# Kernel optimization log

Hardware: AMD Instinct MI355X
Metric: run time of the kernel (lower is better)

Reference implementation:

```python
import jax, jax.numpy as jnp
import numpy as np

NUM_HEADS = 8
KEY_DIM = 512      # total projected dim across heads
VALUE_DIM = 512
EMBED_DIM = 512


def setup_inputs() -> dict:
    key = jax.random.key(0)
    ks = jax.random.split(key, 12)
    B, S, E = 8, 1024, EMBED_DIM
    sc_in = 1.0 / np.sqrt(E)
    sc_o = 1.0 / np.sqrt(KEY_DIM)
    return {
        "queries": jax.random.normal(ks[0], (B, S, E), jnp.float32),
        "keys": jax.random.normal(ks[1], (B, S, E), jnp.float32),
        "values": jax.random.normal(ks[2], (B, S, E), jnp.float32),
        "Wq": jax.random.normal(ks[3], (E, KEY_DIM), jnp.float32) * sc_in,
        "bq": jnp.zeros((KEY_DIM,), jnp.float32),
        "Wk": jax.random.normal(ks[4], (E, KEY_DIM), jnp.float32) * sc_in,
        "bk": jnp.zeros((KEY_DIM,), jnp.float32),
        "Wv": jax.random.normal(ks[5], (E, VALUE_DIM), jnp.float32) * sc_in,
        "bv": jnp.zeros((VALUE_DIM,), jnp.float32),
        "Wo": jax.random.normal(ks[6], (KEY_DIM, EMBED_DIM), jnp.float32) * sc_o,
        "bo": jnp.zeros((EMBED_DIM,), jnp.float32),
    }


def _split_heads(x):
    # [B, S, key_dim] -> [B, H, S, key_dim//H]
    B, S, D = x.shape
    return x.reshape(B, S, NUM_HEADS, D // NUM_HEADS).transpose(0, 2, 1, 3)


def reference(queries, keys, values, Wq, bq, Wk, bk, Wv, bv, Wo, bo):
    q = _split_heads(queries @ Wq + bq)   # [B,H,S,dh]
    k = _split_heads(keys @ Wk + bk)
    v = _split_heads(values @ Wv + bv)
    # NOTE: original scales by sqrt(full key_dim), not per-head dim
    scores = jnp.einsum("bhqd,bhkd->bhqk", q, k) / jnp.sqrt(
        jnp.asarray(KEY_DIM, jnp.float32))
    weights = jax.nn.softmax(scores, axis=-1)
    o = jnp.einsum("bhqk,bhkd->bhqd", weights, v)  # [B,H,S,dh]
    B, H, S, dh = o.shape
    o = o.transpose(0, 2, 1, 3).reshape(B, S, H * dh)  # merge heads -> key_dim
    return o @ Wo + bo
```

## Files before the change

kernel.cpp:

```cpp
#include <hip/hip_runtime.h>


typedef __bf16 bf16x8 __attribute__((ext_vector_type(8)));
typedef __bf16 bf16x4 __attribute__((ext_vector_type(4)));
typedef float  f32x4  __attribute__((ext_vector_type(4)));

#define MFMA(a, b, c) __builtin_amdgcn_mfma_f32_16x16x32_bf16((a), (b), (c), 0, 0, 0)

#define WAITN_BAR(N) asm volatile("s_waitcnt vmcnt(" #N ")\n\ts_barrier" ::: "memory")

__device__ inline bf16x8 cvt8(const float* p) {
  f32x4 u = *(const f32x4*)p;
  f32x4 v = *(const f32x4*)(p + 4);
  bf16x8 r;
  r[0] = (__bf16)u[0]; r[1] = (__bf16)u[1]; r[2] = (__bf16)u[2]; r[3] = (__bf16)u[3];
  r[4] = (__bf16)v[0]; r[5] = (__bf16)v[1]; r[6] = (__bf16)v[2]; r[7] = (__bf16)v[3];
  return r;
}

__device__ inline void gl_lds(const __bf16* g, __bf16* l) {
  __builtin_amdgcn_global_load_lds((const __attribute__((address_space(1))) void*)g,
                                   (__attribute__((address_space(3))) void*)l, 16, 0, 0);
}

__global__ __launch_bounds__(256) void cvt_qkv(const float* __restrict__ Q,
                                               const float* __restrict__ K,
                                               const float* __restrict__ V,
                                               __bf16* __restrict__ Qo,
                                               __bf16* __restrict__ Ko,
                                               __bf16* __restrict__ Vo) {
  const float* src;
  __bf16* dst;
  switch (blockIdx.y) {
    case 0: src = Q; dst = Qo; break;
    case 1: src = K; dst = Ko; break;
    default: src = V; dst = Vo; break;
  }
  const long idx = ((long)blockIdx.x * 256 + threadIdx.x) * 8;
  *(bf16x8*)(dst + idx) = cvt8(src + idx);
}

__global__ __launch_bounds__(256) void transpose_w4(const float* __restrict__ W0,
                                                    const float* __restrict__ W1,
                                                    const float* __restrict__ W2,
                                                    const float* __restrict__ W3,
                                                    __bf16* __restrict__ O0,
                                                    __bf16* __restrict__ O1,
                                                    __bf16* __restrict__ O2,
                                                    __bf16* __restrict__ O3,
                                                    float s0) {
  const float* in;
  __bf16* out;
  float sc = 1.0f;
  switch (blockIdx.y) {
    case 0: in = W0; out = O0; sc = s0; break;
    case 1: in = W1; out = O1; break;
    case 2: in = W2; out = O2; break;
    default: in = W3; out = O3; break;
  }
  __shared__ __align__(16) float t[64][65];
  const int tk = (blockIdx.x & 7) * 64;
  const int tn = (blockIdx.x >> 3) * 64;
  const int r0 = threadIdx.x >> 4;
  const int c4 = threadIdx.x & 15;
#pragma unroll
  for (int i = 0; i < 4; ++i) {
    int r = r0 + i * 16;
    f32x4 v = *(const f32x4*)(in + (long)(tk + r) * 512 + tn + c4 * 4);
#pragma unroll
    for (int j = 0; j < 4; ++j) t[r][c4 * 4 + j] = v[j] * sc;
  }
  __syncthreads();
  const int n0 = threadIdx.x >> 3;
  const int k8 = threadIdx.x & 7;
#pragma unroll
  for (int i = 0; i < 2; ++i) {
    int n = n0 + i * 32;
    bf16x8 v;
#pragma unroll
    for (int j = 0; j < 8; ++j) v[j] = (__bf16)t[k8 * 8 + j][n];
    *(bf16x8*)(out + (long)(tn + n) * 512 + tk + k8 * 8) = v;
  }
}

template <int MODE, typename OT>
__device__ __forceinline__ void gemm_core(const __bf16* __restrict__ X,
                                          const __bf16* __restrict__ Wt,
                                          const float* __restrict__ bias,
                                          OT* __restrict__ out, float bsc,
                                          char* smem) {
  __bf16* At = (__bf16*)smem;
  __bf16* Bt = (__bf16*)(smem + 24576);

  const int tid = threadIdx.x;
  const int lane = tid & 63, wid = tid >> 6, quad = lane >> 4, l16 = lane & 15;
  const int i = blockIdx.x;
  const int kk = i >> 3;
  const int bm = ((i & 7) * 8 + (kk >> 2)) * 128;
  const int bn = (kk & 3) * 128;
  const int wm = (wid >> 1) * 64;
  const int wn = (wid & 1) * 64;

  f32x4 acc[4][4] = {};

  const int rowB = lane >> 2;
  const int gB = (lane & 3) ^ ((rowB >> 1) & 3);

  auto stage = [&](int off, int k0) {
#pragma unroll
    for (int j = 0; j < 2; ++j) {
      const int g = wid * 2 + j;
      gl_lds(X + (long)(bm + g * 16 + rowB) * 512 + k0 + (gB << 3),
             &At[off + g * 512 + lane * 8]);
      gl_lds(Wt + (long)(bn + g * 16 + rowB) * 512 + k0 + (gB << 3),
             &Bt[off + g * 512 + lane * 8]);
    }
  };

  const int posm = quad ^ ((l16 >> 1) & 3);

  auto compute = [&](int co) {
    bf16x8 a[4], b[4];
#pragma unroll
    for (int t = 0; t < 4; ++t) {
      a[t] = *(const bf16x8*)(&At[co + (wm + t * 16 + l16) * 32 + (posm << 3)]);
      b[t] = *(const bf16x8*)(&Bt[co + (wn + t * 16 + l16) * 32 + (posm << 3)]);
    }
#pragma unroll
    for (int mt = 0; mt < 4; ++mt)
#pragma unroll
      for (int nt = 0; nt < 4; ++nt) acc[mt][nt] = MFMA(a[mt], b[nt], acc[mt][nt]);
  };

  stage(0, 0);
  stage(4096, 32);

  int co = 0, so = 8192;
  for (int c = 0; c < 15; ++c) {
    WAITN_BAR(4);
    if (c < 14) stage(so, (c + 2) * 32);
    compute(co);
    const int nc = 12288 - co - so;
    so = co;
    co = nc;
  }
  WAITN_BAR(0);
  compute(co);

  if constexpr (MODE == 4) {
    __syncthreads();
    __bf16* tb = (__bf16*)smem;
#pragma unroll
    for (int nt = 0; nt < 4; ++nt) {
      const int n = wn + nt * 16 + l16;
      const float bvv = bias[bn + n] * bsc;
#pragma unroll
      for (int mt = 0; mt < 4; ++mt) {
        const int m0 = wm + mt * 16 + quad * 4;
        bf16x4 w;
#pragma unroll
        for (int r = 0; r < 4; ++r) w[r] = (__bf16)(acc[mt][nt][r] + bvv);
        *(bf16x4*)(&tb[n * 128 + (((m0 >> 3) ^ (n & 15)) << 3) + (m0 & 7)]) = w;
      }
    }
    __syncthreads();
    const int nn = tid & 127, mhalf = tid >> 7;
    const int d = nn & 63, h = (bn + nn) >> 6;
    const int bb = bm >> 10;
    OT* ob = out + (long)(bb * 8 + h) * 65536;
#pragma unroll
    for (int gi = 0; gi < 8; ++gi) {
      const int gl = mhalf * 8 + gi;
      bf16x8 v = *(const bf16x8*)(&tb[nn * 128 + ((gl ^ (nn & 15)) << 3)]);
      const int cidx = ((bm & 1023) + (gl << 3)) >> 6;
      *(bf16x8*)(ob + cidx * 4096 + d * 64 + ((gi ^ (d & 7)) << 3)) = v;
    }
    return;
  }

#pragma unroll
  for (int nt = 0; nt < 4; ++nt) {
    const int n = bn + wn + nt * 16 + l16;
    const float bvv = bias[n] * bsc;
    const int h = n >> 6, d = n & 63;
#pragma unroll
    for (int mt = 0; mt < 4; ++mt) {
#pragma unroll
      for (int r = 0; r < 4; ++r) {
        const int m = bm + wm + mt * 16 + quad * 4 + r;
        const float v = acc[mt][nt][r] + bvv;
        if constexpr (MODE == 0) {
          out[(long)m * 512 + n] = (OT)v;
        } else if constexpr (MODE == 1) {
          const int bb = m >> 10, s = m & 1023;
          out[((long)((bb * 8 + h) * 1024 + s)) * 64 + d] = (OT)v;
        } else {
          const int bb = m >> 10, s = m & 1023;
          const long idx = (long)(bb * 8 + h) * 65536 + (s >> 6) * 4096 +
                           (s & 63) * 64 + (((d >> 3) ^ (s & 7)) << 3) + (d & 7);
          out[idx] = (OT)v;
        }
      }
    }
  }
}

__global__ __launch_bounds__(256) void gemm_qkv(
    const __bf16* __restrict__ Qx, const __bf16* __restrict__ Kx,
    const __bf16* __restrict__ Vx, const __bf16* __restrict__ Wqt,
    const __bf16* __restrict__ Wkt, const __bf16* __restrict__ Wvt,
    const float* __restrict__ bq, const float* __restrict__ bk,
    const float* __restrict__ bv, __bf16* __restrict__ Qp,
    __bf16* __restrict__ Kp, __bf16* __restrict__ Vtp, float qscale) {
  __shared__ __align__(16) char smem[49152];
  if (blockIdx.y == 0)
    gemm_core<1, __bf16>(Qx, Wqt, bq, Qp, qscale, smem);
  else if (blockIdx.y == 1)
    gemm_core<3, __bf16>(Kx, Wkt, bk, Kp, 1.0f, smem);
  else
    gemm_core<4, __bf16>(Vx, Wvt, bv, Vtp, 1.0f, smem);
}

__global__ __launch_bounds__(256) void gemm_o(const __bf16* __restrict__ Oc,
                                              const __bf16* __restrict__ Wot,
                                              const float* __restrict__ bo,
                                              float* __restrict__ out) {
  __shared__ __align__(16) char smem[49152];
  gemm_core<0, float>(Oc, Wot, bo, out, 1.0f, smem);
}

__global__ __launch_bounds__(256) void attn(const __bf16* __restrict__ Q,
                                            const __bf16* __restrict__ K,
                                            const __bf16* __restrict__ Vt,
                                            __bf16* __restrict__ Oc) {
  __shared__ __align__(16) __bf16 kbuf[12288];
  __shared__ __align__(16) __bf16 vbuf[12288];
  __shared__ __align__(16) __bf16 plds[4][2048];

  const int tid = threadIdx.x;
  const int lane = tid & 63, wid = tid >> 6, quad = lane >> 4, l16 = lane & 15;
  const int i = blockIdx.x;
  const int pair = (i & 7) + (((i >> 6) & 7) << 3);
  const int qt = (i >> 3) & 7;
  const int q0 = qt * 128 + wid * 32;
  const int b = pair >> 3, h = pair & 7;
  const int swz = l16 & 7;

  const __bf16* Qb = Q + (long)pair * 65536;
  const __bf16* Kb = K + (long)pair * 65536;
  const __bf16* Vb = Vt + (long)pair * 65536;
  __bf16* pw = plds[wid];

  bf16x8 bq[2][2];
#pragma unroll
  for (int t = 0; t < 2; ++t)
#pragma unroll
    for (int e = 0; e < 2; ++e)
      bq[t][e] = *(const bf16x8*)(Qb + (q0 + t * 16 + l16) * 64 + e * 32 + quad * 8);
  asm volatile("s_waitcnt vmcnt(0)" ::: "memory");

  float lr[2] = {0.f, 0.f};
  f32x4 oa[2][4] = {};

  auto stage = [&](int off, int c_) {
    const __bf16* kg = Kb + c_ * 4096 + tid * 8;
    const __bf16* vg = Vb + c_ * 4096 + tid * 8;
    gl_lds(kg, &kbuf[off + tid * 8]);
    gl_lds(kg + 2048, &kbuf[off + 2048 + tid * 8]);
    gl_lds(vg, &vbuf[off + tid * 8]);
    gl_lds(vg + 2048, &vbuf[off + 2048 + tid * 8]);
  };

  auto body = [&](int co) {
    f32x4 s[2][4] = {};
#pragma unroll
    for (int kt = 0; kt < 4; ++kt) {
      const int krow = co + (kt * 16 + l16) * 64;
      bf16x8 a0 = *(const bf16x8*)(&kbuf[krow + ((quad ^ swz) << 3)]);
      bf16x8 a1 = *(const bf16x8*)(&kbuf[krow + (((4 + quad) ^ swz) << 3)]);
#pragma unroll
      for (int t = 0; t < 2; ++t) {
        s[t][kt] = MFMA(a0, bq[t][0], s[t][kt]);
        s[t][kt] = MFMA(a1, bq[t][1], s[t][kt]);
      }
    }

#pragma unroll
    for (int t = 0; t < 2; ++t) {
      const int prow = (t * 16 + l16) * 64;
#pragma unroll
      for (int kt = 0; kt < 4; ++kt) {
        bf16x4 w;
#pragma unroll
        for (int r = 0; r < 4; ++r) {
          const float p = exp2f(s[t][kt][r]);
          lr[t] += p;
          w[r] = (__bf16)p;
        }
        *(bf16x4*)(&pw[prow + (((kt * 2 + (quad >> 1)) ^ swz) << 3) + (quad & 1) * 4]) = w;
      }
    }
    bf16x8 pb[2][2];
#pragma unroll
    for (int t = 0; t < 2; ++t)
#pragma unroll
      for (int e = 0; e < 2; ++e)
        pb[t][e] = *(const bf16x8*)(&pw[(t * 16 + l16) * 64 + (((e * 4 + quad) ^ swz) << 3)]);

#pragma unroll
    for (int nt = 0; nt < 4; ++nt) {
      const int drow = co + (nt * 16 + l16) * 64;
      bf16x8 v0 = *(const bf16x8*)(&vbuf[drow + ((quad ^ swz) << 3)]);
      bf16x8 v1 = *(const bf16x8*)(&vbuf[drow + (((4 + quad) ^ swz) << 3)]);
#pragma unroll
      for (int t = 0; t < 2; ++t) {
        oa[t][nt] = MFMA(v0, pb[t][0], oa[t][nt]);
        oa[t][nt] = MFMA(v1, pb[t][1], oa[t][nt]);
      }
    }
  };

  stage(0, 0);
  stage(4096, 1);

  int co = 0, so = 8192;
  for (int c = 0; c < 15; ++c) {
    WAITN_BAR(4);
    if (c < 14) stage(so, c + 2);
    body(co);
    const int nc = 12288 - co - so;
    so = co;
    co = nc;
  }
  WAITN_BAR(0);
  body(co);

#pragma unroll
  for (int t = 0; t < 2; ++t) {
    lr[t] += __shfl_xor(lr[t], 16);
    lr[t] += __shfl_xor(lr[t], 32);
    const float inv = 1.0f / lr[t];
    const long base = ((long)b * 1024 + q0 + t * 16 + l16) * 512 + h * 64 + quad * 4;
#pragma unroll
    for (int nt = 0; nt < 4; ++nt) {
      bf16x4 w;
#pragma unroll
      for (int r = 0; r < 4; ++r) w[r] = (__bf16)(oa[t][nt][r] * inv);
      *(bf16x4*)(Oc + base + nt * 16) = w;
    }
  }
}

extern "C" void kernel_launch(void* const* d_in, const int* in_sizes, int n_in,
                              void* d_out, int out_size, void* d_ws, size_t ws_size,
                              hipStream_t stream) {
  const float* queries = (const float*)d_in[0];
  const float* keys = (const float*)d_in[1];
  const float* values = (const float*)d_in[2];
  const float* Wq = (const float*)d_in[3];
  const float* bq = (const float*)d_in[4];
  const float* Wk = (const float*)d_in[5];
  const float* bk = (const float*)d_in[6];
  const float* Wv = (const float*)d_in[7];
  const float* bv = (const float*)d_in[8];
  const float* Wo = (const float*)d_in[9];
  const float* bo = (const float*)d_in[10];
  float* out = (float*)d_out;

  __bf16* ws = (__bf16*)d_ws;
  const long WSZ = 512 * 512;
  const long XSZ = 8192L * 512;
  __bf16* Wqt = ws;
  __bf16* Wkt = ws + WSZ;
  __bf16* Wvt = ws + 2 * WSZ;
  __bf16* Wot = ws + 3 * WSZ;
  __bf16* Qp = ws + 4 * WSZ;
  __bf16* Kp = Qp + XSZ;
  __bf16* Vtp = Kp + XSZ;
  __bf16* Oc = Vtp + XSZ;
  __bf16* Qbf = Oc + XSZ;
  __bf16* Kbf = Qbf + XSZ;
  __bf16* Vbf = Kbf + XSZ;

  const float qscale = 0.044194173824159216f * 1.4426950408889634f;

  cvt_qkv<<<dim3(2048, 3), 256, 0, stream>>>(queries, keys, values, Qbf, Kbf, Vbf);
  transpose_w4<<<dim3(64, 4), 256, 0, stream>>>(Wq, Wk, Wv, Wo, Wqt, Wkt, Wvt, Wot,
                                                qscale);

  gemm_qkv<<<dim3(256, 3), 256, 0, stream>>>(Qbf, Kbf, Vbf, Wqt, Wkt, Wvt,
                                             bq, bk, bv, Qp, Kp, Vtp, qscale);

  attn<<<512, 256, 0, stream>>>(Qp, Kp, Vtp, Oc);

  gemm_o<<<256, 256, 0, stream>>>(Oc, Wot, bo, out);
}
```

Measured before the change: 181.6 us.

## Store K/V in MFMA fragment layout and load directly to registers in attention

The K and V projection epilogues now write data pre-arranged in MFMA fragment order, so each lane can read its operand fragments from global memory with contiguous 16-byte loads. The attention kernel drops the LDS staging, the barriers and the triple buffering for K/V, and instead double-buffers K fragments in registers and loads V per chunk. It also uses the raw v_exp_f32 instruction, vector row-sum accumulators, s_setprio around MFMA blocks, and a launch bound of two blocks per CU. The cost is more register pressure, and every wave reads K/V from global or L2 on its own, with no sharing through LDS across the block.

```diff
diff --git a/kernel.cpp b/kernel.cpp
--- a/kernel.cpp
+++ b/kernel.cpp
@@ -8,6 +8,12 @@
 #define MFMA(a, b, c) __builtin_amdgcn_mfma_f32_16x16x32_bf16((a), (b), (c), 0, 0, 0)
 
 #define WAITN_BAR(N) asm volatile("s_waitcnt vmcnt(" #N ")\n\ts_barrier" ::: "memory")
+
+__device__ inline float fast_exp2(float x) {
+  float r;
+  asm("v_exp_f32 %0, %1" : "=v"(r) : "v"(x));
+  return r;
+}
 
 __device__ inline bf16x8 cvt8(const float* p) {
   f32x4 u = *(const f32x4*)p;
@@ -165,15 +171,17 @@
     }
     __syncthreads();
     const int nn = tid & 127, mhalf = tid >> 7;
-    const int d = nn & 63, h = (bn + nn) >> 6;
+    const int h = (bn + nn) >> 6;
     const int bb = bm >> 10;
     OT* ob = out + (long)(bb * 8 + h) * 65536;
+    const int cbase = (bm & 1023) >> 6;
 #pragma unroll
     for (int gi = 0; gi < 8; ++gi) {
       const int gl = mhalf * 8 + gi;
       bf16x8 v = *(const bf16x8*)(&tb[nn * 128 + ((gl ^ (nn & 15)) << 3)]);
-      const int cidx = ((bm & 1023) + (gl << 3)) >> 6;
-      *(bf16x8*)(ob + cidx * 4096 + d * 64 + ((gi ^ (d & 7)) << 3)) = v;
+      const long idx = ((((long)(cbase + (gl >> 3)) * 4 + ((nn >> 4) & 3)) * 2 +
+                        ((gl >> 2) & 1)) * 64 + (gl & 3) * 16 + (nn & 15)) * 8;
+      *(bf16x8*)(ob + idx) = v;
     }
     return;
   }
@@ -196,8 +204,9 @@
           out[((long)((bb * 8 + h) * 1024 + s)) * 64 + d] = (OT)v;
         } else {
           const int bb = m >> 10, s = m & 1023;
-          const long idx = (long)(bb * 8 + h) * 65536 + (s >> 6) * 4096 +
-                           (s & 63) * 64 + (((d >> 3) ^ (s & 7)) << 3) + (d & 7);
+          const long idx = (long)(bb * 8 + h) * 65536 +
+                           ((((s >> 6) * 4 + ((s >> 4) & 3)) * 2 + (d >> 5)) * 64 +
+                            ((d >> 3) & 3) * 16 + (s & 15)) * 8 + (d & 7);
           out[idx] = (OT)v;
         }
       }
@@ -229,12 +238,10 @@
   gemm_core<0, float>(Oc, Wot, bo, out, 1.0f, smem);
 }
 
-__global__ __launch_bounds__(256) void attn(const __bf16* __restrict__ Q,
-                                            const __bf16* __restrict__ K,
-                                            const __bf16* __restrict__ Vt,
-                                            __bf16* __restrict__ Oc) {
-  __shared__ __align__(16) __bf16 kbuf[12288];
-  __shared__ __align__(16) __bf16 vbuf[12288];
+__global__ __launch_bounds__(256, 2) void attn(const __bf16* __restrict__ Q,
+                                               const __bf16* __restrict__ Kf,
+                                               const __bf16* __restrict__ Vf,
+                                               __bf16* __restrict__ Oc) {
   __shared__ __align__(16) __bf16 plds[4][2048];
 
   const int tid = threadIdx.x;
@@ -247,8 +254,8 @@
   const int swz = l16 & 7;
 
   const __bf16* Qb = Q + (long)pair * 65536;
-  const __bf16* Kb = K + (long)pair * 65536;
-  const __bf16* Vb = Vt + (long)pair * 65536;
+  const __bf16* Kb = Kf + (long)pair * 65536 + lane * 8;
+  const __bf16* Vb = Vf + (long)pair * 65536 + lane * 8;
   __bf16* pw = plds[wid];
 
   bf16x8 bq[2][2];
@@ -257,89 +264,77 @@
 #pragma unroll
     for (int e = 0; e < 2; ++e)
       bq[t][e] = *(const bf16x8*)(Qb + (q0 + t * 16 + l16) * 64 + e * 32 + quad * 8);
-  asm volatile("s_waitcnt vmcnt(0)" ::: "memory");
-
-  float lr[2] = {0.f, 0.f};
+
+  f32x4 lrv[2] = {};
   f32x4 oa[2][4] = {};
 
-  auto stage = [&](int off, int c_) {
-    const __bf16* kg = Kb + c_ * 4096 + tid * 8;
-    const __bf16* vg = Vb + c_ * 4096 + tid * 8;
-    gl_lds(kg, &kbuf[off + tid * 8]);
-    gl_lds(kg + 2048, &kbuf[off + 2048 + tid * 8]);
-    gl_lds(vg, &vbuf[off + tid * 8]);
-    gl_lds(vg + 2048, &vbuf[off + 2048 + tid * 8]);
-  };
-
-  auto body = [&](int co) {
-    f32x4 s[2][4] = {};
-#pragma unroll
-    for (int kt = 0; kt < 4; ++kt) {
-      const int krow = co + (kt * 16 + l16) * 64;
-      bf16x8 a0 = *(const bf16x8*)(&kbuf[krow + ((quad ^ swz) << 3)]);
-      bf16x8 a1 = *(const bf16x8*)(&kbuf[krow + (((4 + quad) ^ swz) << 3)]);
-#pragma unroll
-      for (int t = 0; t < 2; ++t) {
-        s[t][kt] = MFMA(a0, bq[t][0], s[t][kt]);
-        s[t][kt] = MFMA(a1, bq[t][1], s[t][kt]);
-      }
-    }
-
-#pragma unroll
-    for (int t = 0; t < 2; ++t) {
-      const int prow = (t * 16 + l16) * 64;
-#pragma unroll
-      for (int kt = 0; kt < 4; ++kt) {
-        bf16x4 w;
-#pragma unroll
-        for (int r = 0; r < 4; ++r) {
-          const float p = exp2f(s[t][kt][r]);
-          lr[t] += p;
-          w[r] = (__bf16)p;
-        }
-        *(bf16x4*)(&pw[prow + (((kt * 2 + (quad >> 1)) ^ swz) << 3) + (quad & 1) * 4]) = w;
-      }
-    }
-    bf16x8 pb[2][2];
-#pragma unroll
-    for (int t = 0; t < 2; ++t)
-#pragma unroll
-      for (int e = 0; e < 2; ++e)
-        pb[t][e] = *(const bf16x8*)(&pw[(t * 16 + l16) * 64 + (((e * 4 + quad) ^ swz) << 3)]);
-
-#pragma unroll
-    for (int nt = 0; nt < 4; ++nt) {
-      const int drow = co + (nt * 16 + l16) * 64;
-      bf16x8 v0 = *(const bf16x8*)(&vbuf[drow + ((quad ^ swz) << 3)]);
-      bf16x8 v1 = *(const bf16x8*)(&vbuf[drow + (((4 + quad) ^ swz) << 3)]);
-#pragma unroll
-      for (int t = 0; t < 2; ++t) {
-        oa[t][nt] = MFMA(v0, pb[t][0], oa[t][nt]);
-        oa[t][nt] = MFMA(v1, pb[t][1], oa[t][nt]);
-      }
-    }
-  };
-
-  stage(0, 0);
-  stage(4096, 1);
-
-  int co = 0, so = 8192;
-  for (int c = 0; c < 15; ++c) {
-    WAITN_BAR(4);
-    if (c < 14) stage(so, c + 2);
-    body(co);
-    const int nc = 12288 - co - so;
-    so = co;
-    co = nc;
-  }
-  WAITN_BAR(0);
-  body(co);
+#define LOADK(dst, cc)                                                         \
+  {                                                                            \
+    _Pragma("unroll") for (int kt = 0; kt < 4; ++kt)                           \
+        _Pragma("unroll") for (int e = 0; e < 2; ++e)                          \
+            dst[kt][e] =                                                       \
+        *(const bf16x8*)(Kb + ((((cc) * 4 + kt) * 2 + e) << 9));               \
+  }
+
+#define ABODY(kcur, knxt, cc)                                                  \
+  {                                                                            \
+    bf16x8 vf[4][2];                                                           \
+    _Pragma("unroll") for (int nt = 0; nt < 4; ++nt)                           \
+        _Pragma("unroll") for (int e = 0; e < 2; ++e)                          \
+            vf[nt][e] =                                                        \
+        *(const bf16x8*)(Vb + ((((cc) * 4 + nt) * 2 + e) << 9));               \
+    f32x4 s[2][4] = {};                                                        \
+    __builtin_amdgcn_s_setprio(1);                                             \
+    _Pragma("unroll") for (int kt = 0; kt < 4; ++kt)                           \
+        _Pragma("unroll") for (int t = 0; t < 2; ++t) {                        \
+      s[t][kt] = MFMA(kcur[kt][0], bq[t][0], s[t][kt]);                        \
+      s[t][kt] = MFMA(kcur[kt][1], bq[t][1], s[t][kt]);                        \
+    }                                                                          \
+    __builtin_amdgcn_s_setprio(0);                                             \
+    if ((cc) < 15) LOADK(knxt, (cc) + 1);                                      \
+    _Pragma("unroll") for (int t = 0; t < 2; ++t) {                            \
+      const int prow = (t * 16 + l16) * 64;                                    \
+      _Pragma("unroll") for (int kt = 0; kt < 4; ++kt) {                       \
+        bf16x4 w;                                                              \
+        _Pragma("unroll") for (int r = 0; r < 4; ++r) {                        \
+          const float p = fast_exp2(s[t][kt][r]);                              \
+          lrv[t][r] += p;                                                      \
+          w[r] = (__bf16)p;                                                    \
+        }                                                                      \
+        *(bf16x4*)(&pw[prow + (((kt * 2 + (quad >> 1)) ^ swz) << 3) +          \
+                       (quad & 1) * 4]) = w;                                   \
+      }                                                                        \
+    }                                                                          \
+    bf16x8 pb[2][2];                                                           \
+    _Pragma("unroll") for (int t = 0; t < 2; ++t)                              \
+        _Pragma("unroll") for (int e = 0; e < 2; ++e)                          \
+            pb[t][e] = *(const bf16x8*)(&pw[(t * 16 + l16) * 64 +              \
+                                            (((e * 4 + quad) ^ swz) << 3)]);   \
+    __builtin_amdgcn_s_setprio(1);                                             \
+    _Pragma("unroll") for (int nt = 0; nt < 4; ++nt)                           \
+        _Pragma("unroll") for (int t = 0; t < 2; ++t) {                        \
+      oa[t][nt] = MFMA(vf[nt][0], pb[t][0], oa[t][nt]);                        \
+      oa[t][nt] = MFMA(vf[nt][1], pb[t][1], oa[t][nt]);                        \
+    }                                                                          \
+    __builtin_amdgcn_s_setprio(0);                                             \
+  }
+
+  bf16x8 kA[4][2], kB[4][2];
+  LOADK(kA, 0);
+#pragma unroll 1
+  for (int c = 0; c < 16; c += 2) {
+    ABODY(kA, kB, c);
+    ABODY(kB, kA, c + 1);
+  }
+#undef LOADK
+#undef ABODY
 
 #pragma unroll
   for (int t = 0; t < 2; ++t) {
-    lr[t] += __shfl_xor(lr[t], 16);
-    lr[t] += __shfl_xor(lr[t], 32);
-    const float inv = 1.0f / lr[t];
+    float lr = lrv[t][0] + lrv[t][1] + lrv[t][2] + lrv[t][3];
+    lr += __shfl_xor(lr, 16);
+    lr += __shfl_xor(lr, 32);
+    const float inv = 1.0f / lr;
     const long base = ((long)b * 1024 + q0 + t * 16 + l16) * 512 + h * 64 + quad * 4;
 #pragma unroll
     for (int nt = 0; nt < 4; ++nt) {
```

New measurement: 162.1 us. 1.12x faster.
